# Kernel tuning notes

Measured on AMD Instinct MI355X. Metric: run time of the kernel, lower is better.

Reference implementation:

```python
import jax, jax.numpy as jnp
import numpy as np
import math

D = 768
H = 12
DFF = 3072
HD = D // H


def _layernorm(x, g, b, eps=1e-5):
    mu = jnp.mean(x, axis=-1, keepdims=True)
    var = jnp.var(x, axis=-1, keepdims=True)
    return (x - mu) * jax.lax.rsqrt(var + eps) * g + b


def setup_inputs() -> dict:
    key = jax.random.key(0)
    ks = jax.random.split(key, 12)
    B, S = 2, 4096
    s = 1.0 / math.sqrt(D)
    sf = 1.0 / math.sqrt(DFF)
    return {
        "x": jax.random.normal(ks[0], (B, S, D), jnp.float32),
        "attention_mask": jnp.ones((B, S), jnp.int32),
        "ln1_g": jnp.ones((D,), jnp.float32),
        "ln1_b": jnp.zeros((D,), jnp.float32),
        "ln2_g": jnp.ones((D,), jnp.float32),
        "ln2_b": jnp.zeros((D,), jnp.float32),
        "Wq": jax.random.normal(ks[1], (D, D), jnp.float32) * s,
        "bq": jnp.zeros((D,), jnp.float32),
        "Wk": jax.random.normal(ks[2], (D, D), jnp.float32) * s,
        "bk": jnp.zeros((D,), jnp.float32),
        "Wv": jax.random.normal(ks[3], (D, D), jnp.float32) * s,
        "bv": jnp.zeros((D,), jnp.float32),
        "Wo": jax.random.normal(ks[4], (D, D), jnp.float32) * s,
        "bo": jnp.zeros((D,), jnp.float32),
        "W1": jax.random.normal(ks[5], (D, DFF), jnp.float32) * s,
        "b1": jnp.zeros((DFF,), jnp.float32),
        "W2": jax.random.normal(ks[6], (DFF, D), jnp.float32) * sf,
        "b2": jnp.zeros((D,), jnp.float32),
    }


def _block(x, attention_mask, ln1_g, ln1_b, ln2_g, ln2_b,
           Wq, bq, Wk, bk, Wv, bv, Wo, bo, W1, b1, W2, b2):
    B, S, _ = x.shape
    h = _layernorm(x, ln1_g, ln1_b)
    q = (h @ Wq + bq).reshape(B, S, H, HD)
    k = (h @ Wk + bk).reshape(B, S, H, HD)
    v = (h @ Wv + bv).reshape(B, S, H, HD)
    # scores: [B, H, S, S]
    dots = jnp.einsum('bqhd,bkhd->bhqk', q, k) / math.sqrt(HD)
    causal = jnp.tril(jnp.ones((S, S), bool))  # True = keep
    keep = causal[None, None] & (attention_mask != 0)[:, None, None, :]
    dots = jnp.where(keep, dots, -jnp.inf)
    probs = jax.nn.softmax(dots, axis=-1)
    ctx = jnp.einsum('bhqk,bkhd->bqhd', probs, v).reshape(B, S, D)
    sa = ctx @ Wo + bo  # dropout = identity (eval)
    x = x + sa
    h2 = _layernorm(x, ln2_g, ln2_b)
    ff = jax.nn.relu(h2 @ W1 + b1) @ W2 + b2
    return x + ff


def reference(x, attention_mask, ln1_g, ln1_b, ln2_g, ln2_b,
              Wq, bq, Wk, bk, Wv, bv, Wo, bo, W1, b1, W2, b2):
    return _block(x, attention_mask, ln1_g, ln1_b, ln2_g, ln2_b,
                  Wq, bq, Wk, bk, Wv, bv, Wo, bo, W1, b1, W2, b2)
```

## Files before the change

### kernel.cpp

```cpp
#include <hip/hip_runtime.h>
#include <hip/hip_bf16.h>
#include <math.h>

#define S_LEN 4096
#define DMODEL 768
#define NHEAD 12
#define HDIM 64
#define DFF_ 3072
#define MROWS 8192

typedef __bf16 bf16;
typedef __bf16 bf16x4 __attribute__((ext_vector_type(4)));
typedef __bf16 bf16x8 __attribute__((ext_vector_type(8)));
typedef float f32x4 __attribute__((ext_vector_type(4)));
typedef short s16x4 __attribute__((ext_vector_type(4)));

union F4 { float4 v; float f[4]; };
union U2 { bf16 h[2]; unsigned u; };
union U8 { unsigned u[4]; bf16x8 v; };

#if __has_builtin(__builtin_amdgcn_mfma_f32_16x16x16bf16_1k)
typedef s16x4 mf16_t;
#define MFMA16(a, b, c) __builtin_amdgcn_mfma_f32_16x16x16bf16_1k((a), (b), (c), 0, 0, 0)
#define HAVE_MFMA16 1
#elif __has_builtin(__builtin_amdgcn_mfma_f32_16x16x16_bf16)
typedef bf16x4 mf16_t;
#define MFMA16(a, b, c) __builtin_amdgcn_mfma_f32_16x16x16_bf16((a), (b), (c), 0, 0, 0)
#define HAVE_MFMA16 1
#else
#define HAVE_MFMA16 0
#endif

#if HAVE_MFMA16
union U4 { unsigned u[2]; mf16_t v; };
#endif

__device__ __forceinline__ void gld_lds16(void* lds, const void* g) {
    __builtin_amdgcn_global_load_lds(
        (const __attribute__((address_space(1))) unsigned int*)g,
        (__attribute__((address_space(3))) unsigned int*)lds, 16, 0, 0);
}

template<typename OUT>
__global__ __launch_bounds__(256) void ln_kernel(const float* __restrict__ x,
                                                 const float* __restrict__ g,
                                                 const float* __restrict__ bta,
                                                 OUT* __restrict__ out,
                                                 float* __restrict__ zb) {
    const int row = blockIdx.x;
    const int t = threadIdx.x;
    if (zb && row == 0 && t < 192)
        ((float4*)zb)[t] = make_float4(0.f, 0.f, 0.f, 0.f);
    const float* xr = x + (size_t)row * DMODEL;
    float v0 = xr[t], v1 = xr[t + 256], v2 = xr[t + 512];
    float s = v0 + v1 + v2;
    float ss = v0 * v0 + v1 * v1 + v2 * v2;
    for (int o = 32; o > 0; o >>= 1) {
        s += __shfl_down(s, o, 64);
        ss += __shfl_down(ss, o, 64);
    }
    __shared__ float sm[4], sm2[4];
    const int w = t >> 6, lane = t & 63;
    if (lane == 0) { sm[w] = s; sm2[w] = ss; }
    __syncthreads();
    s = sm[0] + sm[1] + sm[2] + sm[3];
    ss = sm2[0] + sm2[1] + sm2[2] + sm2[3];
    const float mu = s * (1.0f / DMODEL);
    const float var = ss * (1.0f / DMODEL) - mu * mu;
    const float rs = rsqrtf(var + 1e-5f);
    OUT* orow = out + (size_t)row * DMODEL;
    orow[t]       = (OUT)((v0 - mu) * rs * g[t]       + bta[t]);
    orow[t + 256] = (OUT)((v1 - mu) * rs * g[t + 256] + bta[t + 256]);
    orow[t + 512] = (OUT)((v2 - mu) * rs * g[t + 512] + bta[t + 512]);
}

__global__ __launch_bounds__(256) void wtrans_all_kernel(
    const float* __restrict__ Wq, const float* __restrict__ Wk,
    const float* __restrict__ Wv, const float* __restrict__ Wo,
    const float* __restrict__ W1, const float* __restrict__ W2,
    bf16* __restrict__ Wqt, bf16* __restrict__ Wkt, bf16* __restrict__ Wvt,
    bf16* __restrict__ Wot, bf16* __restrict__ W1t, bf16* __restrict__ W2t) {
    int t = blockIdx.x;
    const float* W; bf16* Wt; int K, N;
    if      (t < 144)  { W = Wq; Wt = Wqt; K = 768;  N = 768;  }
    else if (t < 288)  { W = Wk; Wt = Wkt; K = 768;  N = 768;  t -= 144; }
    else if (t < 432)  { W = Wv; Wt = Wvt; K = 768;  N = 768;  t -= 288; }
    else if (t < 576)  { W = Wo; Wt = Wot; K = 768;  N = 768;  t -= 432; }
    else if (t < 1152) { W = W1; Wt = W1t; K = 768;  N = 3072; t -= 576; }
    else               { W = W2; Wt = W2t; K = 3072; N = 768;  t -= 1152; }
    const int nx = N >> 6;
    const int n0 = (t % nx) * 64, k0 = (t / nx) * 64;

    __shared__ float tile[64][65];
    const int tid = threadIdx.x;
    const int lr = tid >> 4, lc = (tid & 15) << 2;
#pragma unroll
    for (int i = 0; i < 4; ++i) {
        const int r = lr + i * 16;
        F4 w; w.v = *(const float4*)&W[(size_t)(k0 + r) * N + n0 + lc];
#pragma unroll
        for (int j = 0; j < 4; ++j) tile[r][lc + j] = w.f[j];
    }
    __syncthreads();
#pragma unroll
    for (int i = 0; i < 4; ++i) {
        const int n = lr + i * 16;
        bf16x4 o;
#pragma unroll
        for (int j = 0; j < 4; ++j) o[j] = (bf16)tile[lc + j][n];
        *(bf16x4*)&Wt[(size_t)(n0 + n) * K + k0 + lc] = o;
    }
}

template<int MT, bool RELU, bool RES, bool OUT_BF16>
__global__ __launch_bounds__(256) void mgemm_kernel(
    const bf16* __restrict__ A,
    const bf16* __restrict__ Wt0, const float* __restrict__ bias0, void* __restrict__ C0,
    const bf16* __restrict__ Wt1, const float* __restrict__ bias1, void* __restrict__ C1,
    const bf16* __restrict__ Wt2, const float* __restrict__ bias2, void* __restrict__ C2,
    const float* __restrict__ R, int M, int N, int K, int Kloop,
    int koff0, int koff1, int koff2,
    float sc0, float sc1, float sc2) {
    const bf16* Wt = Wt0; const float* bias = bias0; void* C = C0; float sc = sc0; int koff = koff0;
    if (blockIdx.z == 1) { Wt = Wt1; bias = bias1; C = C1; sc = sc1; koff = koff1; }
    if (blockIdx.z == 2) { Wt = Wt2; bias = bias2; C = C2; sc = sc2; koff = koff2; }

    constexpr int NI = (MT == 128) ? 4 : 2;
    __shared__ bf16 As[2][MT * 32];
    __shared__ bf16 Bs[2][128 * 32];

    const int tid = threadIdx.x;
    const int wave = tid >> 6, lane = tid & 63;
    const int row0 = blockIdx.y * MT, col0 = blockIdx.x * 128;
    const int wr = (MT == 128) ? (wave >> 1) * 64 : 0;
    const int wc = (MT == 128) ? (wave & 1) * 64 : wave * 32;
    const int mrow = lane & 15, kq = (lane >> 4) * 8;

    const int st_row = (lane >> 2);
    const int st_off = (lane & 3) * 16;

    f32x4 acc[4][NI] = {};

    const char* Ab = (const char*)(A + (size_t)row0 * K + koff);
    const char* Bb = (const char*)(Wt + (size_t)col0 * K + koff);
    const size_t strideA = (size_t)K * 2;

    for (int k0 = 0; k0 < Kloop; k0 += 64) {
#pragma unroll
        for (int s = 0; s < 2; ++s) {
            const int kk = k0 + s * 32;
            if (MT == 128) {
#pragma unroll
                for (int issue = 0; issue < 2; ++issue) {
                    const int r = wave * 32 + issue * 16 + st_row;
                    gld_lds16((char*)As[s] + (wave * 32 + issue * 16) * 64,
                              Ab + (size_t)r * strideA + kk * 2 + st_off);
                }
            } else {
                const int r = wave * 16 + st_row;
                gld_lds16((char*)As[s] + (wave * 16) * 64,
                          Ab + (size_t)r * strideA + kk * 2 + st_off);
            }
#pragma unroll
            for (int issue = 0; issue < 2; ++issue) {
                const int r = wave * 32 + issue * 16 + st_row;
                gld_lds16((char*)Bs[s] + (wave * 32 + issue * 16) * 64,
                          Bb + (size_t)r * strideA + kk * 2 + st_off);
            }
        }
        __syncthreads();
#pragma unroll
        for (int s = 0; s < 2; ++s) {
            bf16x8 af[4], bfr[NI];
#pragma unroll
            for (int mi = 0; mi < 4; ++mi)
                af[mi] = *(const bf16x8*)&As[s][(wr + mi * 16 + mrow) * 32 + kq];
#pragma unroll
            for (int ni = 0; ni < NI; ++ni)
                bfr[ni] = *(const bf16x8*)&Bs[s][(wc + ni * 16 + mrow) * 32 + kq];
#pragma unroll
            for (int mi = 0; mi < 4; ++mi)
#pragma unroll
                for (int ni = 0; ni < NI; ++ni)
                    acc[mi][ni] = __builtin_amdgcn_mfma_f32_16x16x32_bf16(
                        af[mi], bfr[ni], acc[mi][ni], 0, 0, 0);
        }
        __syncthreads();
    }

    const int quad = lane >> 4;
    float bv[NI];
#pragma unroll
    for (int ni = 0; ni < NI; ++ni) bv[ni] = bias[col0 + wc + ni * 16 + mrow];
#pragma unroll
    for (int mi = 0; mi < 4; ++mi) {
#pragma unroll
        for (int r = 0; r < 4; ++r) {
            const int row = row0 + wr + mi * 16 + quad * 4 + r;
#pragma unroll
            for (int ni = 0; ni < NI; ++ni) {
                const int col = col0 + wc + ni * 16 + mrow;
                float v = acc[mi][ni][r] + bv[ni];
                if (RES) v += R[(size_t)row * N + col];
                v *= sc;
                if (RELU) v = fmaxf(v, 0.0f);
                if (OUT_BF16) ((bf16*)C)[(size_t)row * N + col] = (bf16)v;
                else          ((float*)C)[(size_t)row * N + col] = v;
            }
        }
    }
}

__global__ __launch_bounds__(256) void ff2_combine_kernel(
    const bf16* __restrict__ p0, const bf16* __restrict__ p1,
    const float* __restrict__ b2, const float* __restrict__ x1,
    float* __restrict__ out) {
    const int i = (blockIdx.x * 256 + threadIdx.x) * 4;
    bf16x4 a = *(const bf16x4*)(p0 + i);
    bf16x4 b = *(const bf16x4*)(p1 + i);
    F4 xr; xr.v = *(const float4*)(x1 + i);
    const int col = i % DMODEL;
    F4 o;
#pragma unroll
    for (int j = 0; j < 4; ++j)
        o.f[j] = (float)a[j] + (float)b[j] + b2[col + j] + xr.f[j];
    *(float4*)(out + i) = o.v;
}

__global__ __launch_bounds__(256) void mattn_kernel(
    const bf16* __restrict__ Q, const bf16* __restrict__ K,
    const bf16* __restrict__ V, const int* __restrict__ amask,
    bf16* __restrict__ O) {
    const int bx = blockIdx.x, h = blockIdx.y, b = blockIdx.z;

    __shared__ bf16 Ks[2][64][68];
#if HAVE_MFMA16
    __shared__ bf16 Vt[2][80][68];
#else
    __shared__ bf16 Vt[2][64][68];
#endif
    __shared__ bf16 Os[64][68];
    __shared__ float mk[2][64];
    __shared__ int flagv[2];

    const int tid = threadIdx.x;
    const int wave = tid >> 6, lane = tid & 63;
    const int l = lane & 15, quad = lane >> 4;
#if !HAVE_MFMA16
    const int qh = quad >> 1;
    const int srcA = (quad & 1) * 32 + l;
    const int srcB = srcA + 16;
#endif
    const float NEG_INF = -__builtin_huge_valf();

    const int kr = tid >> 2, ks = (tid & 3) * 16;
    const int vk0 = (tid & 31) * 2, vds = (tid >> 5) * 8;

    const bf16* Kbase = K + (size_t)b * S_LEN * DMODEL + h * HDIM;
    const bf16* Vbase = V + (size_t)b * S_LEN * DMODEL + h * HDIM;

#if HAVE_MFMA16
    if (tid < 68) {
        Vt[0][64][tid] = (bf16)1.0f;
        Vt[1][64][tid] = (bf16)1.0f;
    }
#endif

#pragma unroll 1
    for (int pass = 0; pass < 2; ++pass) {
        const int qt = pass ? bx : (63 - bx);

        const bf16* Qb = Q + (size_t)(b * S_LEN + qt * 64 + wave * 16 + l) * DMODEL + h * HDIM;
        const bf16x8 qf0 = *(const bf16x8*)(Qb + quad * 8);
        const bf16x8 qf1 = *(const bf16x8*)(Qb + 32 + quad * 8);

        float m_run = NEG_INF;
#if !HAVE_MFMA16
        float l_run = 0.0f;
#endif
        f32x4 acc[4] = {};
#if HAVE_MFMA16
        f32x4 acc_l = {};
#endif

        bf16x8 kp0, kp1, vp0, vp1;
        int mv = 1;
        {
            const bf16* kg = Kbase + (size_t)kr * DMODEL + ks;
            kp0 = *(const bf16x8*)kg;
            kp1 = *(const bf16x8*)(kg + 8);
            const bf16* vg = Vbase + (size_t)vk0 * DMODEL + vds;
            vp0 = *(const bf16x8*)vg;
            vp1 = *(const bf16x8*)(vg + DMODEL);
            if (wave == 0) mv = amask[b * S_LEN + lane];
        }
        __syncthreads();
        {
            *(bf16x8*)&Ks[0][kr][ks]     = kp0;
            *(bf16x8*)&Ks[0][kr][ks + 8] = kp1;
#pragma unroll
            for (int i = 0; i < 8; ++i) {
                U2 w; w.h[0] = vp0[i]; w.h[1] = vp1[i];
                *(unsigned*)&Vt[0][vds + i][vk0] = w.u;
            }
            if (wave == 0) {
                mk[0][lane] = mv ? 0.0f : NEG_INF;
                unsigned long long bal = __ballot(mv != 0);
                if (lane == 0) flagv[0] = (bal == ~0ULL);
            }
        }
        __syncthreads();
        int buf = 0;

        for (int kt = 0; kt <= qt; ++kt) {
            const bool more = (kt < qt);
            if (more) {
                const bf16* kg = Kbase + (size_t)((kt + 1) * 64 + kr) * DMODEL + ks;
                kp0 = *(const bf16x8*)kg;
                kp1 = *(const bf16x8*)(kg + 8);
                const bf16* vg = Vbase + (size_t)((kt + 1) * 64 + vk0) * DMODEL + vds;
                vp0 = *(const bf16x8*)vg;
                vp1 = *(const bf16x8*)(vg + DMODEL);
                if (wave == 0) mv = amask[b * S_LEN + (kt + 1) * 64 + lane];
            }

            const int allv = flagv[buf];
            f32x4 sreg[4] = {};
#pragma unroll
            for (int mi = 0; mi < 4; ++mi) {
                bf16x8 kf0 = *(const bf16x8*)&Ks[buf][mi * 16 + l][quad * 8];
                bf16x8 kf1 = *(const bf16x8*)&Ks[buf][mi * 16 + l][32 + quad * 8];
                sreg[mi] = __builtin_amdgcn_mfma_f32_16x16x32_bf16(kf0, qf0, sreg[mi], 0, 0, 0);
                sreg[mi] = __builtin_amdgcn_mfma_f32_16x16x32_bf16(kf1, qf1, sreg[mi], 0, 0, 0);
            }
            if (!allv) {
#pragma unroll
                for (int mi = 0; mi < 4; ++mi) {
                    F4 m4; m4.v = *(const float4*)&mk[buf][mi * 16 + quad * 4];
#pragma unroll
                    for (int r = 0; r < 4; ++r) sreg[mi][r] += m4.f[r];
                }
            }
            if (kt == qt) {
#pragma unroll
                for (int mi = 0; mi < 4; ++mi)
#pragma unroll
                    for (int r = 0; r < 4; ++r)
                        if (mi * 16 + quad * 4 + r > wave * 16 + l)
                            sreg[mi][r] = NEG_INF;
            }

            float mloc = sreg[0][0];
#pragma unroll
            for (int mi = 0; mi < 4; ++mi)
#pragma unroll
                for (int r = 0; r < 4; ++r) mloc = fmaxf(mloc, sreg[mi][r]);
            mloc = fmaxf(mloc, __shfl_xor(mloc, 16, 64));
            mloc = fmaxf(mloc, __shfl_xor(mloc, 32, 64));
            const float mn = fmaxf(m_run, mloc);
            const float alpha = __builtin_amdgcn_exp2f(m_run - mn);
            m_run = mn;
#pragma unroll
            for (int mi = 0; mi < 4; ++mi)
#pragma unroll
                for (int r = 0; r < 4; ++r)
                    sreg[mi][r] = __builtin_amdgcn_exp2f(sreg[mi][r] - mn);
#if !HAVE_MFMA16
            float ls = 0.0f;
#pragma unroll
            for (int mi = 0; mi < 4; ++mi)
#pragma unroll
                for (int r = 0; r < 4; ++r) ls += sreg[mi][r];
            ls += __shfl_xor(ls, 16, 64);
            ls += __shfl_xor(ls, 32, 64);
            l_run = l_run * alpha + ls;
#endif
#pragma unroll
            for (int mi = 0; mi < 4; ++mi)
#pragma unroll
                for (int r = 0; r < 4; ++r) acc[mi][r] *= alpha;
#if HAVE_MFMA16
#pragma unroll
            for (int r = 0; r < 4; ++r) acc_l[r] *= alpha;
#endif

            unsigned pk[4][2];
#pragma unroll
            for (int mi = 0; mi < 4; ++mi) {
                U2 w0; w0.h[0] = (bf16)sreg[mi][0]; w0.h[1] = (bf16)sreg[mi][1];
                U2 w1; w1.h[0] = (bf16)sreg[mi][2]; w1.h[1] = (bf16)sreg[mi][3];
                pk[mi][0] = w0.u; pk[mi][1] = w1.u;
            }

#if HAVE_MFMA16
#pragma unroll
            for (int mi = 0; mi < 4; ++mi) {
                U4 pb; pb.u[0] = pk[mi][0]; pb.u[1] = pk[mi][1];
#pragma unroll
                for (int di = 0; di < 4; ++di) {
                    mf16_t va = *(const mf16_t*)&Vt[buf][di * 16 + l][mi * 16 + quad * 4];
                    acc[di] = MFMA16(va, pb.v, acc[di]);
                }
                mf16_t vl = *(const mf16_t*)&Vt[buf][64 + l][mi * 16 + quad * 4];
                acc_l = MFMA16(vl, pb.v, acc_l);
            }
#else
            bf16x8 pfrag[2];
#pragma unroll
            for (int kc = 0; kc < 2; ++kc) {
                U8 u;
#pragma unroll
                for (int t = 0; t < 2; ++t) {
                    const unsigned a0 = (unsigned)__shfl((int)pk[2 * kc][t],     srcA, 64);
                    const unsigned b0 = (unsigned)__shfl((int)pk[2 * kc + 1][t], srcA, 64);
                    u.u[t] = qh ? b0 : a0;
                    const unsigned a1 = (unsigned)__shfl((int)pk[2 * kc][t],     srcB, 64);
                    const unsigned b1 = (unsigned)__shfl((int)pk[2 * kc + 1][t], srcB, 64);
                    u.u[2 + t] = qh ? b1 : a1;
                }
                pfrag[kc] = u.v;
            }
#pragma unroll
            for (int mi = 0; mi < 4; ++mi) {
                bf16x8 vf0 = *(const bf16x8*)&Vt[buf][mi * 16 + l][quad * 8];
                bf16x8 vf1 = *(const bf16x8*)&Vt[buf][mi * 16 + l][32 + quad * 8];
                acc[mi] = __builtin_amdgcn_mfma_f32_16x16x32_bf16(vf0, pfrag[0], acc[mi], 0, 0, 0);
                acc[mi] = __builtin_amdgcn_mfma_f32_16x16x32_bf16(vf1, pfrag[1], acc[mi], 0, 0, 0);
            }
#endif

            if (more) {
                const int nb = buf ^ 1;
                *(bf16x8*)&Ks[nb][kr][ks]     = kp0;
                *(bf16x8*)&Ks[nb][kr][ks + 8] = kp1;
#pragma unroll
                for (int i = 0; i < 8; ++i) {
                    U2 w; w.h[0] = vp0[i]; w.h[1] = vp1[i];
                    *(unsigned*)&Vt[nb][vds + i][vk0] = w.u;
                }
                if (wave == 0) {
                    mk[nb][lane] = mv ? 0.0f : NEG_INF;
                    unsigned long long bal = __ballot(mv != 0);
                    if (lane == 0) flagv[nb] = (bal == ~0ULL);
                }
            }
            __syncthreads();
            buf ^= 1;
        }

#if HAVE_MFMA16
        const float l_run = __shfl(acc_l[0], l, 64);
#endif
        const float rinv = 1.0f / l_run;
#pragma unroll
        for (int mi = 0; mi < 4; ++mi) {
            U2 w0; w0.h[0] = (bf16)(acc[mi][0] * rinv); w0.h[1] = (bf16)(acc[mi][1] * rinv);
            U2 w1; w1.h[0] = (bf16)(acc[mi][2] * rinv); w1.h[1] = (bf16)(acc[mi][3] * rinv);
            *(unsigned*)&Os[wave * 16 + l][mi * 16 + quad * 4]     = w0.u;
            *(unsigned*)&Os[wave * 16 + l][mi * 16 + quad * 4 + 2] = w1.u;
        }
        __syncthreads();
        {
            const int orow = tid >> 2, oseg = (tid & 3) * 16;
            bf16* Og = O + (size_t)(b * S_LEN + qt * 64 + orow) * DMODEL + h * HDIM + oseg;
            *(bf16x8*)Og       = *(const bf16x8*)&Os[orow][oseg];
            *(bf16x8*)(Og + 8) = *(const bf16x8*)&Os[orow][oseg + 8];
        }
    }
}

extern "C" void kernel_launch(void* const* d_in, const int* in_sizes, int n_in,
                              void* d_out, int out_size, void* d_ws, size_t ws_size,
                              hipStream_t stream) {
    const float* x     = (const float*)d_in[0];
    const int*   amask = (const int*)  d_in[1];
    const float* ln1_g = (const float*)d_in[2];
    const float* ln1_b = (const float*)d_in[3];
    const float* ln2_g = (const float*)d_in[4];
    const float* ln2_b = (const float*)d_in[5];
    const float* Wq = (const float*)d_in[6];  const float* bq = (const float*)d_in[7];
    const float* Wk = (const float*)d_in[8];  const float* bk = (const float*)d_in[9];
    const float* Wv = (const float*)d_in[10]; const float* bv = (const float*)d_in[11];
    const float* Wo = (const float*)d_in[12]; const float* bo = (const float*)d_in[13];
    const float* W1 = (const float*)d_in[14]; const float* b1 = (const float*)d_in[15];
    const float* W2 = (const float*)d_in[16]; const float* b2 = (const float*)d_in[17];
    float* out = (float*)d_out;

    char* ws = (char*)d_ws;
    const size_t WSML = (size_t)DMODEL * DMODEL * 2;
    const size_t WBIG = (size_t)DMODEL * DFF_ * 2;
    bf16* Wqt = (bf16*)(ws + 0 * WSML);
    bf16* Wkt = (bf16*)(ws + 1 * WSML);
    bf16* Wvt = (bf16*)(ws + 2 * WSML);
    bf16* Wot = (bf16*)(ws + 3 * WSML);
    bf16* W1t = (bf16*)(ws + 4 * WSML);
    bf16* W2t = (bf16*)(ws + 4 * WSML + WBIG);
    char* act = ws + 4 * WSML + 2 * WBIG;

    const size_t HB = (size_t)MROWS * DMODEL * 2;
    const size_t FB = (size_t)MROWS * DMODEL * 4;
    bf16*  h    = (bf16*)(act);
    bf16*  qb   = (bf16*)(act + HB);
    bf16*  kb   = (bf16*)(act + 2 * HB);
    bf16*  vb   = (bf16*)(act + 3 * HB);
    bf16*  ctx  = h;
    float* x1   = (float*)(act + 4 * HB);
    bf16*  f    = (bf16*)(act + 4 * HB + FB);
    bf16*  h2   = h;
    bf16*  p0   = qb;
    bf16*  p1   = kb;
    float* zbias = (float*)vb;

    const float SCL = 0.125f * 1.44269504089f;

    wtrans_all_kernel<<<1728, 256, 0, stream>>>(Wq, Wk, Wv, Wo, W1, W2,
                                                Wqt, Wkt, Wvt, Wot, W1t, W2t);

    ln_kernel<bf16><<<MROWS, 256, 0, stream>>>(x, ln1_g, ln1_b, h, nullptr);
    mgemm_kernel<128, false, false, true><<<dim3(DMODEL / 128, MROWS / 128, 3), 256, 0, stream>>>(
        h, Wqt, bq, qb, Wkt, bk, kb, Wvt, bv, vb, nullptr,
        MROWS, DMODEL, DMODEL, DMODEL, 0, 0, 0, SCL, 1.0f, 1.0f);
    mattn_kernel<<<dim3(32, NHEAD, 2), 256, 0, stream>>>(qb, kb, vb, amask, ctx);
    mgemm_kernel<64, false, true, false><<<dim3(DMODEL / 128, MROWS / 64, 1), 256, 0, stream>>>(
        ctx, Wot, bo, x1, Wot, bo, x1, Wot, bo, x1, x,
        MROWS, DMODEL, DMODEL, DMODEL, 0, 0, 0, 1.0f, 1.0f, 1.0f);
    ln_kernel<bf16><<<MROWS, 256, 0, stream>>>(x1, ln2_g, ln2_b, h2, zbias);
    mgemm_kernel<128, true, false, true><<<dim3(DFF_ / 128, MROWS / 128, 1), 256, 0, stream>>>(
        h2, W1t, b1, f, W1t, b1, f, W1t, b1, f, nullptr,
        MROWS, DFF_, DMODEL, DMODEL, 0, 0, 0, 1.0f, 1.0f, 1.0f);
    mgemm_kernel<128, false, false, true><<<dim3(DMODEL / 128, MROWS / 128, 2), 256, 0, stream>>>(
        f, W2t, zbias, p0, W2t, zbias, p1, W2t, zbias, p1, nullptr,
        MROWS, DMODEL, DFF_, DFF_ / 2, 0, DFF_ / 2, 0, 1.0f, 1.0f, 1.0f);
    ff2_combine_kernel<<<(MROWS * DMODEL) / 1024, 256, 0, stream>>>(p0, p1, b2, x1, out);
}
```

Before: 465.2 us.

## Split attention into one query tile per block with lazy rescale and setprio

The attention kernel stops pairing two query tiles per block (long+short) and launches one block per query tile, ordered longest-first, doubling the grid. It also adds a conditional online-softmax rescale that only updates the running max when the new max exceeds it by a threshold, replaces the LDS ones-row for the row-sum MFMA with a register constant, reuses the K buffer for the output staging, and raises wave priority around MFMA blocks. The aim is better load balance and occupancy plus fewer exp/scale ops, at the cost of less explicit work balancing per block and reliance on the hardware scheduler ordering.

After: 518.5 us. 11.5% more time.

```diff
diff --git a/kernel.cpp b/kernel.cpp
--- a/kernel.cpp
+++ b/kernel.cpp
@@ -231,15 +231,11 @@
     const bf16* __restrict__ Q, const bf16* __restrict__ K,
     const bf16* __restrict__ V, const int* __restrict__ amask,
     bf16* __restrict__ O) {
-    const int bx = blockIdx.x, h = blockIdx.y, b = blockIdx.z;
+    const int qt = 63 - blockIdx.x;
+    const int h = blockIdx.y, b = blockIdx.z;
 
     __shared__ bf16 Ks[2][64][68];
-#if HAVE_MFMA16
-    __shared__ bf16 Vt[2][80][68];
-#else
     __shared__ bf16 Vt[2][64][68];
-#endif
-    __shared__ bf16 Os[64][68];
     __shared__ float mk[2][64];
     __shared__ int flagv[2];
 
@@ -260,212 +256,212 @@
     const bf16* Vbase = V + (size_t)b * S_LEN * DMODEL + h * HDIM;
 
 #if HAVE_MFMA16
-    if (tid < 68) {
-        Vt[0][64][tid] = (bf16)1.0f;
-        Vt[1][64][tid] = (bf16)1.0f;
-    }
-#endif
-
-#pragma unroll 1
-    for (int pass = 0; pass < 2; ++pass) {
-        const int qt = pass ? bx : (63 - bx);
-
-        const bf16* Qb = Q + (size_t)(b * S_LEN + qt * 64 + wave * 16 + l) * DMODEL + h * HDIM;
-        const bf16x8 qf0 = *(const bf16x8*)(Qb + quad * 8);
-        const bf16x8 qf1 = *(const bf16x8*)(Qb + 32 + quad * 8);
-
-        float m_run = NEG_INF;
+    U4 onesf;
+    onesf.u[0] = 0x3F803F80u; onesf.u[1] = 0x3F803F80u;
+#endif
+
+    const bf16* Qb = Q + (size_t)(b * S_LEN + qt * 64 + wave * 16 + l) * DMODEL + h * HDIM;
+    const bf16x8 qf0 = *(const bf16x8*)(Qb + quad * 8);
+    const bf16x8 qf1 = *(const bf16x8*)(Qb + 32 + quad * 8);
+
+    float m_run = NEG_INF;
 #if !HAVE_MFMA16
-        float l_run = 0.0f;
-#endif
-        f32x4 acc[4] = {};
+    float l_run = 0.0f;
+#endif
+    f32x4 acc[4] = {};
 #if HAVE_MFMA16
-        f32x4 acc_l = {};
-#endif
-
-        bf16x8 kp0, kp1, vp0, vp1;
-        int mv = 1;
-        {
-            const bf16* kg = Kbase + (size_t)kr * DMODEL + ks;
+    f32x4 acc_l = {};
+#endif
+
+    bf16x8 kp0, kp1, vp0, vp1;
+    int mv = 1;
+    {
+        const bf16* kg = Kbase + (size_t)kr * DMODEL + ks;
+        kp0 = *(const bf16x8*)kg;
+        kp1 = *(const bf16x8*)(kg + 8);
+        const bf16* vg = Vbase + (size_t)vk0 * DMODEL + vds;
+        vp0 = *(const bf16x8*)vg;
+        vp1 = *(const bf16x8*)(vg + DMODEL);
+        if (wave == 0) mv = amask[b * S_LEN + lane];
+        *(bf16x8*)&Ks[0][kr][ks]     = kp0;
+        *(bf16x8*)&Ks[0][kr][ks + 8] = kp1;
+#pragma unroll
+        for (int i = 0; i < 8; ++i) {
+            U2 w; w.h[0] = vp0[i]; w.h[1] = vp1[i];
+            *(unsigned*)&Vt[0][vds + i][vk0] = w.u;
+        }
+        if (wave == 0) {
+            mk[0][lane] = mv ? 0.0f : NEG_INF;
+            unsigned long long bal = __ballot(mv != 0);
+            if (lane == 0) flagv[0] = (bal == ~0ULL);
+        }
+    }
+    __syncthreads();
+    int buf = 0;
+
+    for (int kt = 0; kt <= qt; ++kt) {
+        const bool more = (kt < qt);
+        if (more) {
+            const bf16* kg = Kbase + (size_t)((kt + 1) * 64 + kr) * DMODEL + ks;
             kp0 = *(const bf16x8*)kg;
             kp1 = *(const bf16x8*)(kg + 8);
-            const bf16* vg = Vbase + (size_t)vk0 * DMODEL + vds;
+            const bf16* vg = Vbase + (size_t)((kt + 1) * 64 + vk0) * DMODEL + vds;
             vp0 = *(const bf16x8*)vg;
             vp1 = *(const bf16x8*)(vg + DMODEL);
-            if (wave == 0) mv = amask[b * S_LEN + lane];
-        }
-        __syncthreads();
-        {
-            *(bf16x8*)&Ks[0][kr][ks]     = kp0;
-            *(bf16x8*)&Ks[0][kr][ks + 8] = kp1;
-#pragma unroll
-            for (int i = 0; i < 8; ++i) {
-                U2 w; w.h[0] = vp0[i]; w.h[1] = vp1[i];
-                *(unsigned*)&Vt[0][vds + i][vk0] = w.u;
-            }
-            if (wave == 0) {
-                mk[0][lane] = mv ? 0.0f : NEG_INF;
-                unsigned long long bal = __ballot(mv != 0);
-                if (lane == 0) flagv[0] = (bal == ~0ULL);
-            }
-        }
-        __syncthreads();
-        int buf = 0;
-
-        for (int kt = 0; kt <= qt; ++kt) {
-            const bool more = (kt < qt);
-            if (more) {
-                const bf16* kg = Kbase + (size_t)((kt + 1) * 64 + kr) * DMODEL + ks;
-                kp0 = *(const bf16x8*)kg;
-                kp1 = *(const bf16x8*)(kg + 8);
-                const bf16* vg = Vbase + (size_t)((kt + 1) * 64 + vk0) * DMODEL + vds;
-                vp0 = *(const bf16x8*)vg;
-                vp1 = *(const bf16x8*)(vg + DMODEL);
-                if (wave == 0) mv = amask[b * S_LEN + (kt + 1) * 64 + lane];
-            }
-
-            const int allv = flagv[buf];
-            f32x4 sreg[4] = {};
+            if (wave == 0) mv = amask[b * S_LEN + (kt + 1) * 64 + lane];
+        }
+
+        const int allv = flagv[buf];
+        f32x4 sreg[4] = {};
+        __builtin_amdgcn_s_setprio(1);
+#pragma unroll
+        for (int mi = 0; mi < 4; ++mi) {
+            bf16x8 kf0 = *(const bf16x8*)&Ks[buf][mi * 16 + l][quad * 8];
+            bf16x8 kf1 = *(const bf16x8*)&Ks[buf][mi * 16 + l][32 + quad * 8];
+            sreg[mi] = __builtin_amdgcn_mfma_f32_16x16x32_bf16(kf0, qf0, sreg[mi], 0, 0, 0);
+            sreg[mi] = __builtin_amdgcn_mfma_f32_16x16x32_bf16(kf1, qf1, sreg[mi], 0, 0, 0);
+        }
+        __builtin_amdgcn_s_setprio(0);
+        if (!allv) {
 #pragma unroll
             for (int mi = 0; mi < 4; ++mi) {
-                bf16x8 kf0 = *(const bf16x8*)&Ks[buf][mi * 16 + l][quad * 8];
-                bf16x8 kf1 = *(const bf16x8*)&Ks[buf][mi * 16 + l][32 + quad * 8];
-                sreg[mi] = __builtin_amdgcn_mfma_f32_16x16x32_bf16(kf0, qf0, sreg[mi], 0, 0, 0);
-                sreg[mi] = __builtin_amdgcn_mfma_f32_16x16x32_bf16(kf1, qf1, sreg[mi], 0, 0, 0);
-            }
-            if (!allv) {
-#pragma unroll
-                for (int mi = 0; mi < 4; ++mi) {
-                    F4 m4; m4.v = *(const float4*)&mk[buf][mi * 16 + quad * 4];
-#pragma unroll
-                    for (int r = 0; r < 4; ++r) sreg[mi][r] += m4.f[r];
-                }
-            }
-            if (kt == qt) {
-#pragma unroll
-                for (int mi = 0; mi < 4; ++mi)
-#pragma unroll
-                    for (int r = 0; r < 4; ++r)
-                        if (mi * 16 + quad * 4 + r > wave * 16 + l)
-                            sreg[mi][r] = NEG_INF;
-            }
-
-            float mloc = sreg[0][0];
+                F4 m4; m4.v = *(const float4*)&mk[buf][mi * 16 + quad * 4];
+#pragma unroll
+                for (int r = 0; r < 4; ++r) sreg[mi][r] += m4.f[r];
+            }
+        }
+        if (kt == qt) {
 #pragma unroll
             for (int mi = 0; mi < 4; ++mi)
 #pragma unroll
-                for (int r = 0; r < 4; ++r) mloc = fmaxf(mloc, sreg[mi][r]);
-            mloc = fmaxf(mloc, __shfl_xor(mloc, 16, 64));
-            mloc = fmaxf(mloc, __shfl_xor(mloc, 32, 64));
+                for (int r = 0; r < 4; ++r)
+                    if (mi * 16 + quad * 4 + r > wave * 16 + l)
+                        sreg[mi][r] = NEG_INF;
+        }
+
+        float mloc = sreg[0][0];
+#pragma unroll
+        for (int mi = 0; mi < 4; ++mi)
+#pragma unroll
+            for (int r = 0; r < 4; ++r) mloc = fmaxf(mloc, sreg[mi][r]);
+        mloc = fmaxf(mloc, __shfl_xor(mloc, 16, 64));
+        mloc = fmaxf(mloc, __shfl_xor(mloc, 32, 64));
+        if (__any(mloc > m_run + 8.0f)) {
             const float mn = fmaxf(m_run, mloc);
             const float alpha = __builtin_amdgcn_exp2f(m_run - mn);
             m_run = mn;
 #pragma unroll
             for (int mi = 0; mi < 4; ++mi)
 #pragma unroll
-                for (int r = 0; r < 4; ++r)
-                    sreg[mi][r] = __builtin_amdgcn_exp2f(sreg[mi][r] - mn);
-#if !HAVE_MFMA16
-            float ls = 0.0f;
-#pragma unroll
-            for (int mi = 0; mi < 4; ++mi)
-#pragma unroll
-                for (int r = 0; r < 4; ++r) ls += sreg[mi][r];
-            ls += __shfl_xor(ls, 16, 64);
-            ls += __shfl_xor(ls, 32, 64);
-            l_run = l_run * alpha + ls;
-#endif
-#pragma unroll
-            for (int mi = 0; mi < 4; ++mi)
-#pragma unroll
                 for (int r = 0; r < 4; ++r) acc[mi][r] *= alpha;
 #if HAVE_MFMA16
 #pragma unroll
             for (int r = 0; r < 4; ++r) acc_l[r] *= alpha;
-#endif
-
-            unsigned pk[4][2];
-#pragma unroll
-            for (int mi = 0; mi < 4; ++mi) {
-                U2 w0; w0.h[0] = (bf16)sreg[mi][0]; w0.h[1] = (bf16)sreg[mi][1];
-                U2 w1; w1.h[0] = (bf16)sreg[mi][2]; w1.h[1] = (bf16)sreg[mi][3];
-                pk[mi][0] = w0.u; pk[mi][1] = w1.u;
-            }
+#else
+            l_run *= alpha;
+#endif
+        }
+#pragma unroll
+        for (int mi = 0; mi < 4; ++mi)
+#pragma unroll
+            for (int r = 0; r < 4; ++r)
+                sreg[mi][r] = __builtin_amdgcn_exp2f(sreg[mi][r] - m_run);
+#if !HAVE_MFMA16
+        float ls = 0.0f;
+#pragma unroll
+        for (int mi = 0; mi < 4; ++mi)
+#pragma unroll
+            for (int r = 0; r < 4; ++r) ls += sreg[mi][r];
+        ls += __shfl_xor(ls, 16, 64);
+        ls += __shfl_xor(ls, 32, 64);
+        l_run += ls;
+#endif
+
+        unsigned pk[4][2];
+#pragma unroll
+        for (int mi = 0; mi < 4; ++mi) {
+            U2 w0; w0.h[0] = (bf16)sreg[mi][0]; w0.h[1] = (bf16)sreg[mi][1];
+            U2 w1; w1.h[0] = (bf16)sreg[mi][2]; w1.h[1] = (bf16)sreg[mi][3];
+            pk[mi][0] = w0.u; pk[mi][1] = w1.u;
+        }
 
 #if HAVE_MFMA16
-#pragma unroll
-            for (int mi = 0; mi < 4; ++mi) {
-                U4 pb; pb.u[0] = pk[mi][0]; pb.u[1] = pk[mi][1];
-#pragma unroll
-                for (int di = 0; di < 4; ++di) {
-                    mf16_t va = *(const mf16_t*)&Vt[buf][di * 16 + l][mi * 16 + quad * 4];
-                    acc[di] = MFMA16(va, pb.v, acc[di]);
-                }
-                mf16_t vl = *(const mf16_t*)&Vt[buf][64 + l][mi * 16 + quad * 4];
-                acc_l = MFMA16(vl, pb.v, acc_l);
-            }
+        __builtin_amdgcn_s_setprio(1);
+#pragma unroll
+        for (int mi = 0; mi < 4; ++mi) {
+            U4 pb; pb.u[0] = pk[mi][0]; pb.u[1] = pk[mi][1];
+#pragma unroll
+            for (int di = 0; di < 4; ++di) {
+                mf16_t va = *(const mf16_t*)&Vt[buf][di * 16 + l][mi * 16 + quad * 4];
+                acc[di] = MFMA16(va, pb.v, acc[di]);
+            }
+            acc_l = MFMA16(onesf.v, pb.v, acc_l);
+        }
+        __builtin_amdgcn_s_setprio(0);
 #else
-            bf16x8 pfrag[2];
-#pragma unroll
-            for (int kc = 0; kc < 2; ++kc) {
-                U8 u;
-#pragma unroll
-                for (int t = 0; t < 2; ++t) {
-                    const unsigned a0 = (unsigned)__shfl((int)pk[2 * kc][t],     srcA, 64);
-                    const unsigned b0 = (unsigned)__shfl((int)pk[2 * kc + 1][t], srcA, 64);
-                    u.u[t] = qh ? b0 : a0;
-                    const unsigned a1 = (unsigned)__shfl((int)pk[2 * kc][t],     srcB, 64);
-                    const unsigned b1 = (unsigned)__shfl((int)pk[2 * kc + 1][t], srcB, 64);
-                    u.u[2 + t] = qh ? b1 : a1;
-                }
-                pfrag[kc] = u.v;
-            }
-#pragma unroll
-            for (int mi = 0; mi < 4; ++mi) {
-                bf16x8 vf0 = *(const bf16x8*)&Vt[buf][mi * 16 + l][quad * 8];
-                bf16x8 vf1 = *(const bf16x8*)&Vt[buf][mi * 16 + l][32 + quad * 8];
-                acc[mi] = __builtin_amdgcn_mfma_f32_16x16x32_bf16(vf0, pfrag[0], acc[mi], 0, 0, 0);
-                acc[mi] = __builtin_amdgcn_mfma_f32_16x16x32_bf16(vf1, pfrag[1], acc[mi], 0, 0, 0);
-            }
-#endif
-
-            if (more) {
-                const int nb = buf ^ 1;
-                *(bf16x8*)&Ks[nb][kr][ks]     = kp0;
-                *(bf16x8*)&Ks[nb][kr][ks + 8] = kp1;
-#pragma unroll
-                for (int i = 0; i < 8; ++i) {
-                    U2 w; w.h[0] = vp0[i]; w.h[1] = vp1[i];
-                    *(unsigned*)&Vt[nb][vds + i][vk0] = w.u;
-                }
-                if (wave == 0) {
-                    mk[nb][lane] = mv ? 0.0f : NEG_INF;
-                    unsigned long long bal = __ballot(mv != 0);
-                    if (lane == 0) flagv[nb] = (bal == ~0ULL);
-                }
-            }
-            __syncthreads();
-            buf ^= 1;
-        }
+        bf16x8 pfrag[2];
+#pragma unroll
+        for (int kc = 0; kc < 2; ++kc) {
+            U8 u;
+#pragma unroll
+            for (int t = 0; t < 2; ++t) {
+                const unsigned a0 = (unsigned)__shfl((int)pk[2 * kc][t],     srcA, 64);
+                const unsigned b0 = (unsigned)__shfl((int)pk[2 * kc + 1][t], srcA, 64);
+                u.u[t] = qh ? b0 : a0;
+                const unsigned a1 = (unsigned)__shfl((int)pk[2 * kc][t],     srcB, 64);
+                const unsigned b1 = (unsigned)__shfl((int)pk[2 * kc + 1][t], srcB, 64);
+                u.u[2 + t] = qh ? b1 : a1;
+            }
+            pfrag[kc] = u.v;
+        }
+#pragma unroll
+        for (int mi = 0; mi < 4; ++mi) {
+            bf16x8 vf0 = *(const bf16x8*)&Vt[buf][mi * 16 + l][quad * 8];
+            bf16x8 vf1 = *(const bf16x8*)&Vt[buf][mi * 16 + l][32 + quad * 8];
+            acc[mi] = __builtin_amdgcn_mfma_f32_16x16x32_bf16(vf0, pfrag[0], acc[mi], 0, 0, 0);
+            acc[mi] = __builtin_amdgcn_mfma_f32_16x16x32_bf16(vf1, pfrag[1], acc[mi], 0, 0, 0);
+        }
+#endif
+
+        if (more) {
+            const int nb = buf ^ 1;
+            *(bf16x8*)&Ks[nb][kr][ks]     = kp0;
+            *(bf16x8*)&Ks[nb][kr][ks + 8] = kp1;
+#pragma unroll
+            for (int i = 0; i < 8; ++i) {
+                U2 w; w.h[0] = vp0[i]; w.h[1] = vp1[i];
+                *(unsigned*)&Vt[nb][vds + i][vk0] = w.u;
+            }
+            if (wave == 0) {
+                mk[nb][lane] = mv ? 0.0f : NEG_INF;
+                unsigned long long bal = __ballot(mv != 0);
+                if (lane == 0) flagv[nb] = (bal == ~0ULL);
+            }
+        }
+        __syncthreads();
+        buf ^= 1;
+    }
 
 #if HAVE_MFMA16
-        const float l_run = __shfl(acc_l[0], l, 64);
-#endif
-        const float rinv = 1.0f / l_run;
-#pragma unroll
-        for (int mi = 0; mi < 4; ++mi) {
-            U2 w0; w0.h[0] = (bf16)(acc[mi][0] * rinv); w0.h[1] = (bf16)(acc[mi][1] * rinv);
-            U2 w1; w1.h[0] = (bf16)(acc[mi][2] * rinv); w1.h[1] = (bf16)(acc[mi][3] * rinv);
-            *(unsigned*)&Os[wave * 16 + l][mi * 16 + quad * 4]     = w0.u;
-            *(unsigned*)&Os[wave * 16 + l][mi * 16 + quad * 4 + 2] = w1.u;
-        }
-        __syncthreads();
-        {
-            const int orow = tid >> 2, oseg = (tid & 3) * 16;
-            bf16* Og = O + (size_t)(b * S_LEN + qt * 64 + orow) * DMODEL + h * HDIM + oseg;
-            *(bf16x8*)Og       = *(const bf16x8*)&Os[orow][oseg];
-            *(bf16x8*)(Og + 8) = *(const bf16x8*)&Os[orow][oseg + 8];
-        }
+    const float l_fin = __shfl(acc_l[0], l, 64);
+#else
+    const float l_fin = l_run;
+#endif
+    const float rinv = 1.0f / l_fin;
+    bf16 (*Os)[68] = (bf16 (*)[68])(&Ks[0][0][0]);
+#pragma unroll
+    for (int mi = 0; mi < 4; ++mi) {
+        U2 w0; w0.h[0] = (bf16)(acc[mi][0] * rinv); w0.h[1] = (bf16)(acc[mi][1] * rinv);
+        U2 w1; w1.h[0] = (bf16)(acc[mi][2] * rinv); w1.h[1] = (bf16)(acc[mi][3] * rinv);
+        *(unsigned*)&Os[wave * 16 + l][mi * 16 + quad * 4]     = w0.u;
+        *(unsigned*)&Os[wave * 16 + l][mi * 16 + quad * 4 + 2] = w1.u;
+    }
+    __syncthreads();
+    {
+        const int orow = tid >> 2, oseg = (tid & 3) * 16;
+        bf16* Og = O + (size_t)(b * S_LEN + qt * 64 + orow) * DMODEL + h * HDIM + oseg;
+        *(bf16x8*)Og       = *(const bf16x8*)&Os[orow][oseg];
+        *(bf16x8*)(Og + 8) = *(const bf16x8*)&Os[orow][oseg + 8];
     }
 }
 
@@ -520,7 +516,7 @@
     mgemm_kernel<128, false, false, true><<<dim3(DMODEL / 128, MROWS / 128, 3), 256, 0, stream>>>(
         h, Wqt, bq, qb, Wkt, bk, kb, Wvt, bv, vb, nullptr,
         MROWS, DMODEL, DMODEL, DMODEL, 0, 0, 0, SCL, 1.0f, 1.0f);
-    mattn_kernel<<<dim3(32, NHEAD, 2), 256, 0, stream>>>(qb, kb, vb, amask, ctx);
+    mattn_kernel<<<dim3(64, NHEAD, 2), 256, 0, stream>>>(qb, kb, vb, amask, ctx);
     mgemm_kernel<64, false, true, false><<<dim3(DMODEL / 128, MROWS / 64, 1), 256, 0, stream>>>(
         ctx, Wot, bo, x1, Wot, bo, x1, Wot, bo, x1, x,
         MROWS, DMODEL, DMODEL, DMODEL, 0, 0, 0, 1.0f, 1.0f, 1.0f);
```

## Remap GEMM workgroups for XCD locality and fuse FF2 epilogue, drop split-K

Applied to the files above, without the earlier changes.

Adds a workgroup index remap in the GEMM kernel that groups consecutive tiles onto the same XCD (lid&7 interleave), aiming to improve L2 reuse of A/B tiles. Replaces the split-K FF2 GEMM (two bf16 partials plus a combine kernel) with a single full-K GEMM using 64-row tiles, with bias and residual fused directly into the float output. This removes the partial-sum write/read traffic and one launch, but gives up the extra parallelism split-K provided, and partials are no longer rounded to bf16.

Result: no change. 460.1 us (-1.1%).

```diff
diff --git a/kernel.cpp b/kernel.cpp
--- a/kernel.cpp
+++ b/kernel.cpp
@@ -125,13 +125,19 @@
     if (blockIdx.z == 1) { Wt = Wt1; bias = bias1; C = C1; sc = sc1; koff = koff1; }
     if (blockIdx.z == 2) { Wt = Wt2; bias = bias2; C = C2; sc = sc2; koff = koff2; }
 
+    const int gx = gridDim.x;
+    const int nwg = gx * gridDim.y;
+    const int chunk = nwg >> 3;
+    int lid = blockIdx.y * gx + blockIdx.x;
+    lid = (lid & 7) * chunk + (lid >> 3);
+    const int row0 = (lid / gx) * MT, col0 = (lid % gx) * 128;
+
     constexpr int NI = (MT == 128) ? 4 : 2;
     __shared__ bf16 As[2][MT * 32];
     __shared__ bf16 Bs[2][128 * 32];
 
     const int tid = threadIdx.x;
     const int wave = tid >> 6, lane = tid & 63;
-    const int row0 = blockIdx.y * MT, col0 = blockIdx.x * 128;
     const int wr = (MT == 128) ? (wave >> 1) * 64 : 0;
     const int wc = (MT == 128) ? (wave & 1) * 64 : wave * 32;
     const int mrow = lane & 15, kq = (lane >> 4) * 8;
@@ -209,22 +215,6 @@
             }
         }
     }
-}
-
-__global__ __launch_bounds__(256) void ff2_combine_kernel(
-    const bf16* __restrict__ p0, const bf16* __restrict__ p1,
-    const float* __restrict__ b2, const float* __restrict__ x1,
-    float* __restrict__ out) {
-    const int i = (blockIdx.x * 256 + threadIdx.x) * 4;
-    bf16x4 a = *(const bf16x4*)(p0 + i);
-    bf16x4 b = *(const bf16x4*)(p1 + i);
-    F4 xr; xr.v = *(const float4*)(x1 + i);
-    const int col = i % DMODEL;
-    F4 o;
-#pragma unroll
-    for (int j = 0; j < 4; ++j)
-        o.f[j] = (float)a[j] + (float)b[j] + b2[col + j] + xr.f[j];
-    *(float4*)(out + i) = o.v;
 }
 
 __global__ __launch_bounds__(256) void mattn_kernel(
@@ -507,9 +497,6 @@
     float* x1   = (float*)(act + 4 * HB);
     bf16*  f    = (bf16*)(act + 4 * HB + FB);
     bf16*  h2   = h;
-    bf16*  p0   = qb;
-    bf16*  p1   = kb;
-    float* zbias = (float*)vb;
 
     const float SCL = 0.125f * 1.44269504089f;
 
@@ -524,12 +511,11 @@
     mgemm_kernel<64, false, true, false><<<dim3(DMODEL / 128, MROWS / 64, 1), 256, 0, stream>>>(
         ctx, Wot, bo, x1, Wot, bo, x1, Wot, bo, x1, x,
         MROWS, DMODEL, DMODEL, DMODEL, 0, 0, 0, 1.0f, 1.0f, 1.0f);
-    ln_kernel<bf16><<<MROWS, 256, 0, stream>>>(x1, ln2_g, ln2_b, h2, zbias);
+    ln_kernel<bf16><<<MROWS, 256, 0, stream>>>(x1, ln2_g, ln2_b, h2, nullptr);
     mgemm_kernel<128, true, false, true><<<dim3(DFF_ / 128, MROWS / 128, 1), 256, 0, stream>>>(
         h2, W1t, b1, f, W1t, b1, f, W1t, b1, f, nullptr,
         MROWS, DFF_, DMODEL, DMODEL, 0, 0, 0, 1.0f, 1.0f, 1.0f);
-    mgemm_kernel<128, false, false, true><<<dim3(DMODEL / 128, MROWS / 128, 2), 256, 0, stream>>>(
-        f, W2t, zbias, p0, W2t, zbias, p1, W2t, zbias, p1, nullptr,
-        MROWS, DMODEL, DFF_, DFF_ / 2, 0, DFF_ / 2, 0, 1.0f, 1.0f, 1.0f);
-    ff2_combine_kernel<<<(MROWS * DMODEL) / 1024, 256, 0, stream>>>(p0, p1, b2, x1, out);
+    mgemm_kernel<64, false, true, false><<<dim3(DMODEL / 128, MROWS / 64, 1), 256, 0, stream>>>(
+        f, W2t, b2, out, W2t, b2, out, W2t, b2, out, x1,
+        MROWS, DMODEL, DFF_, DFF_, 0, 0, 0, 1.0f, 1.0f, 1.0f);
 }
```
